# Kernel tuning notes

Hardware: AMD Instinct MI355X
Metric: run time of the kernel (lower is better)

## Reference

```python
import jax, jax.numpy as jnp
import numpy as np

EPS = 1e-05

def exp_map_at_origin(v, c):
    sqrt_c = jnp.sqrt(c)
    v_norm = jnp.maximum(jnp.linalg.norm(v, axis=-1, keepdims=True), EPS)
    return (1.0 / sqrt_c) * jnp.tanh(sqrt_c * v_norm) * (v / v_norm)

def log_map_at_origin(y, c):
    sqrt_c = jnp.sqrt(c)
    y_norm = jnp.maximum(jnp.linalg.norm(y, axis=-1, keepdims=True), EPS)
    y_norm_clamped = jnp.minimum(y_norm, 1.0 / sqrt_c - EPS)
    return (1.0 / sqrt_c) * jnp.arctanh(sqrt_c * y_norm_clamped) * (y / y_norm)

def poincare_distance(x, y, c):
    # x, y: [B, H, S, d]; returns [B, H, S, S]
    sqrt_c = jnp.sqrt(c)
    xns = jnp.sum(x * x, axis=-1, keepdims=True)          # [B,H,S,1]
    yns = jnp.sum(y * y, axis=-1, keepdims=True)          # [B,H,S,1]
    xy = jnp.einsum('bhsd,bhtd->bhst', x, y)
    xnsb = xns                                            # broadcast over t
    ynsb = jnp.swapaxes(yns, -2, -1)                      # [B,H,1,S]
    diff_norm_sq = xnsb - 2.0 * xy + ynsb
    denom = jnp.maximum((1.0 - c * xnsb) * (1.0 - c * ynsb), EPS)
    arg = jnp.maximum(1.0 + 2.0 * c * diff_norm_sq / denom, 1.0 + EPS)
    return (1.0 / sqrt_c) * jnp.arccosh(arg)

def setup_inputs() -> dict:
    key = jax.random.key(0)
    ks = jax.random.split(key, 5)
    B, S, D = 2, 1024, 1024
    x = jax.random.normal(ks[0], (B, S, D), dtype=jnp.float32)
    scale = 0.02
    W_q = scale * jax.random.normal(ks[1], (D, D), dtype=jnp.float32)
    W_k = scale * jax.random.normal(ks[2], (D, D), dtype=jnp.float32)
    W_v = scale * jax.random.normal(ks[3], (D, D), dtype=jnp.float32)
    W_o = scale * jax.random.normal(ks[4], (D, D), dtype=jnp.float32)
    return {
        'x': x, 'W_q': W_q, 'W_k': W_k, 'W_v': W_v, 'W_o': W_o,
        'log_c': jnp.zeros((), jnp.float32),
        'beta': jnp.zeros((), jnp.float32),
        'attention_bias': jnp.zeros((), jnp.float32),
    }

def reference(x, W_q, W_k, W_v, W_o, log_c, beta, attention_bias):
    B, S, D = x.shape
    H = 16
    dh = D // H
    c = jax.nn.softplus(log_c)
    beta_pos = jax.nn.softplus(beta)

    def split_heads(t):  # [B,S,D] -> [B,H,S,dh]
        return jnp.transpose(t.reshape(B, S, H, dh), (0, 2, 1, 3))

    q_t = split_heads(x @ W_q.T)
    k_t = split_heads(x @ W_k.T)
    v_t = split_heads(x @ W_v.T)

    q_h = exp_map_at_origin(q_t, c)
    k_h = exp_map_at_origin(k_t, c)
    v_h = exp_map_at_origin(v_t, c)

    dist = poincare_distance(q_h, k_h, c)                 # [B,H,S,S]
    scores = -beta_pos * dist - attention_bias
    weights = jax.nn.softmax(scores, axis=-1)

    v_tan = log_map_at_origin(v_h, c)
    out_tan = jnp.einsum('bhst,bhtd->bhsd', weights, v_tan)
    out_hyp = exp_map_at_origin(out_tan, c)
    out_heads_tan = log_map_at_origin(out_hyp, c)

    concat = jnp.transpose(out_heads_tan, (0, 2, 1, 3)).reshape(B, S, D)
    return concat @ W_o.T
```

## Files before the change

kernel.cpp:

```cpp
#include <hip/hip_runtime.h>
#include <math.h>


#define EPS_ 1e-5f

constexpr int Ss = 1024, Dd = 1024, Hh = 16, DHh = 64;

typedef __attribute__((ext_vector_type(8))) short bf16x8;
typedef __attribute__((ext_vector_type(4))) short s16x4;
typedef __attribute__((ext_vector_type(4))) float f32x4;

__device__ __forceinline__ float softplusf_(float x) {
    return (x > 20.f) ? x : log1pf(expf(x));
}
__device__ __forceinline__ short f2bf(float f) {
    union { float f; unsigned u; } v; v.f = f;
    unsigned r = v.u + 0x7FFFu + ((v.u >> 16) & 1u);
    return (short)(r >> 16);
}
__device__ __forceinline__ unsigned pks(short a, short b) {
    return (unsigned)(unsigned short)a | ((unsigned)(unsigned short)b << 16);
}

#if __has_builtin(__builtin_amdgcn_cvt_pk_bf16_f32)
typedef __attribute__((ext_vector_type(2))) __bf16 bfp2;
__device__ __forceinline__ unsigned cvtpk(float a, float b) {
    union { bfp2 v; unsigned u; } x;
    x.v = __builtin_amdgcn_cvt_pk_bf16_f32(a, b);
    return x.u;
}
#else
__device__ __forceinline__ unsigned cvtpk(float a, float b) { return pks(f2bf(a), f2bf(b)); }
#endif

#if __has_builtin(__builtin_amdgcn_sqrtf)
#define FSQRT __builtin_amdgcn_sqrtf
#else
#define FSQRT sqrtf
#endif
#if __has_builtin(__builtin_amdgcn_logf)
#define FLOG2 __builtin_amdgcn_logf
#else
#define FLOG2 __log2f
#endif
#if __has_builtin(__builtin_amdgcn_exp2f)
#define FEXP2 __builtin_amdgcn_exp2f
#else
#define FEXP2 exp2f
#endif

__device__ __forceinline__ void gload_lds16(const short* gp, short* lp) {
    __builtin_amdgcn_global_load_lds(
        (__attribute__((address_space(1))) void*)(void*)(const_cast<short*>(gp)),
        (__attribute__((address_space(3))) void*)(void*)(lp), 16, 0, 0);
}

__global__ __launch_bounds__(256) void split_all(
    const float* __restrict__ x,  const float* __restrict__ Wq,
    const float* __restrict__ Wk, const float* __restrict__ Wv,
    const float* __restrict__ Wo,
    short* __restrict__ xh,  short* __restrict__ wqh,
    short* __restrict__ wkh, short* __restrict__ wvh, short* __restrict__ woh)
{
    int g = blockIdx.x * 256 + threadIdx.x;
    const float* src; short* dst; int base;
    if (g < 524288)       { src = x;  dst = xh;  base = g; }
    else if (g < 786432)  { src = Wq; dst = wqh; base = g - 524288; }
    else if (g < 1048576) { src = Wk; dst = wkh; base = g - 786432; }
    else if (g < 1310720) { src = Wv; dst = wvh; base = g - 1048576; }
    else                  { src = Wo; dst = woh; base = g - 1310720; }
    float4 v = *(const float4*)(src + (size_t)base * 4);
    uint2 hp; hp.x = cvtpk(v.x, v.y); hp.y = cvtpk(v.z, v.w);
    *(uint2*)(dst + (size_t)base * 4) = hp;
}

__global__ __launch_bounds__(256, 3) void gemm_qkv(
    const short* __restrict__ Ap,
    const short* __restrict__ Wq, const short* __restrict__ Wk, const short* __restrict__ Wv,
    short* __restrict__ qh, short* __restrict__ kh, short* __restrict__ vtT,
    float* __restrict__ qnsT, float2* __restrict__ knpk,
    const float* __restrict__ p_logc)
{
    const int z = blockIdx.z;
    const short* Bp = (z == 0) ? Wq : (z == 1 ? Wk : Wv);
    const int K = 1024;

    __shared__ short As[128 * 64];
    __shared__ short Bs[64 * 64];

    const int tid = threadIdx.x;
    const int wv = tid >> 6, lane = tid & 63, quad = lane >> 4, l15 = lane & 15;
    const int bm = blockIdx.y * 128, bn = blockIdx.x * 64;

    const int lr8 = lane >> 3, lc8 = lane & 7;
    const int swz8 = (lc8 ^ lr8) * 8;

    const short* gAl = Ap + (size_t)(bm + lr8) * K + swz8;
    const short* gBl = Bp + (size_t)(bn + lr8) * K + swz8;

    f32x4 acc[2][4];
#pragma unroll
    for (int mt = 0; mt < 2; mt++)
#pragma unroll
        for (int j = 0; j < 4; j++) acc[mt][j] = (f32x4){0.f, 0.f, 0.f, 0.f};

    for (int k0 = 0; k0 < K; k0 += 64) {
        __syncthreads();
#pragma unroll
        for (int i = 0; i < 4; i++)
            gload_lds16(gAl + (size_t)((wv * 4 + i) * 8) * K + k0, &As[(wv * 4 + i) * 512]);
#pragma unroll
        for (int j = 0; j < 2; j++)
            gload_lds16(gBl + (size_t)((wv * 2 + j) * 8) * K + k0, &Bs[(wv * 2 + j) * 512]);
        __syncthreads();
#pragma unroll
        for (int w = 0; w < 2; w++) {
            const int xs = ((w * 4 + quad) ^ (l15 & 7)) * 8;
            bf16x8 fa0 = *(const bf16x8*)&As[(wv * 32 + l15) * 64 + xs];
            bf16x8 fa1 = *(const bf16x8*)&As[(wv * 32 + 16 + l15) * 64 + xs];
#pragma unroll
            for (int nt = 0; nt < 4; nt++) {
                bf16x8 fb = *(const bf16x8*)&Bs[(nt * 16 + l15) * 64 + xs];
                acc[0][nt] = __builtin_amdgcn_mfma_f32_16x16x32_bf16(fa0, fb, acc[0][nt], 0, 0, 0);
                acc[1][nt] = __builtin_amdgcn_mfma_f32_16x16x32_bf16(fa1, fb, acc[1][nt], 0, 0, 0);
            }
        }
    }

    const float c = softplusf_(p_logc[0]);
    const float sc = sqrtf(c);
    const float twoC = 2.f * c;
    const int h0 = blockIdx.x;

    if (z < 2) {
        short* yout = (z == 0) ? qh : kh;
#pragma unroll
        for (int mt = 0; mt < 2; mt++) {
            const int mbase = bm + wv * 32 + mt * 16;
            float fr[4];
#pragma unroll
            for (int r = 0; r < 4; r++) {
                float s2 = 0.f;
#pragma unroll
                for (int nt = 0; nt < 4; nt++) s2 += acc[mt][nt][r] * acc[mt][nt][r];
#pragma unroll
                for (int mk = 1; mk < 16; mk <<= 1) s2 += __shfl_xor(s2, mk, 64);
                float n = fmaxf(sqrtf(s2), EPS_);
                float fac = tanhf(sc * n) / (sc * n);
                fr[r] = fac;
                if (l15 == 0) {
                    int m = mbase + quad * 4 + r;
                    int bI = m >> 10, s = m & 1023;
                    float yns = s2 * fac * fac;
                    if (z == 0) {
                        qnsT[(size_t)(bI * Hh + h0) * Ss + s] = yns;
                    } else {
                        knpk[(size_t)(bI * Hh + h0) * Ss + s]
                            = make_float2(yns, twoC / (1.f - c * yns));
                    }
                }
            }
#pragma unroll
            for (int nt = 0; nt < 4; nt++)
#pragma unroll
                for (int r = 0; r < 4; r++) {
                    int m = mbase + quad * 4 + r;
                    yout[(size_t)m * Dd + bn + nt * 16 + l15] = f2bf(acc[mt][nt][r] * fr[r]);
                }
        }
    } else {
#pragma unroll
        for (int mt = 0; mt < 2; mt++) {
            const int mbase = bm + wv * 32 + mt * 16;
            float tr[4];
#pragma unroll
            for (int r = 0; r < 4; r++) {
                float s2 = 0.f;
#pragma unroll
                for (int nt = 0; nt < 4; nt++) s2 += acc[mt][nt][r] * acc[mt][nt][r];
#pragma unroll
                for (int mk = 1; mk < 16; mk <<= 1) s2 += __shfl_xor(s2, mk, 64);
                float n = fmaxf(sqrtf(s2), EPS_);
                float fac = tanhf(sc * n) / (sc * n);
                float yn = n * fac;
                float ycl = fminf(yn, 1.f / sc - EPS_);
                float f2 = atanhf(sc * ycl) / (sc * fmaxf(yn, EPS_));
                tr[r] = fac * f2;
            }
            const int m0 = mbase + quad * 4;
            const int bI = m0 >> 10, s0 = m0 & 1023;
            const int w6 = s0 & 63;
            const int s0p = (s0 & ~63)
                          | ((w6 >> 5) * 32 + ((w6 & 15) >> 2) * 8 + ((w6 >> 4) & 1) * 4);
#pragma unroll
            for (int nt = 0; nt < 4; nt++) {
                int d = nt * 16 + l15;
                uint2 pk;
                pk.x = cvtpk(acc[mt][nt][0] * tr[0], acc[mt][nt][1] * tr[1]);
                pk.y = cvtpk(acc[mt][nt][2] * tr[2], acc[mt][nt][3] * tr[3]);
                *(uint2*)&vtT[((size_t)(bI * Hh + h0) * DHh + d) * Ss + s0p] = pk;
            }
        }
    }
}

__global__ __launch_bounds__(512) void attn_mfma(
    const short* __restrict__ qh, const short* __restrict__ kh, const short* __restrict__ vtT,
    const float* __restrict__ qnsT, const float2* __restrict__ knpk,
    short* __restrict__ ccb,
    const float* __restrict__ p_logc, const float* __restrict__ p_beta)
{
    const float c = softplusf_(p_logc[0]);
    const float sc = sqrtf(c);
    const float bp = softplusf_(p_beta[0]);
    const float nkc = -bp / sc;
    const float cap = 2.f * c * 1e5f;
    const float onePlus = 1.f + EPS_;

    const int bh = blockIdx.x, qt = blockIdx.y;
    const int b = bh >> 4, h = bh & 15;
    const int tid = threadIdx.x;
    const int wv = tid >> 6, lane = tid & 63;
    const int g = wv >> 2, w4 = wv & 3;
    const int quad = lane >> 4, l15 = lane & 15;
    const int q = qt * 64 + w4 * 16 + l15;

    __shared__ short Ks[2][2][4096];
    __shared__ short Vt[2][2][4096];

    const short* qb = qh + (size_t)(b * Ss + q) * Dd + h * DHh + quad * 8;
    bf16x8 qf0 = *(const bf16x8*)qb;
    bf16x8 qf1 = *(const bf16x8*)(qb + 32);

    const float qn = qnsT[(size_t)bh * Ss + q];
    const float irq = 1.f / (1.f - c * qn);

    f32x4 O4[4];
#pragma unroll
    for (int nt = 0; nt < 4; nt++) O4[nt] = (f32x4){0.f, 0.f, 0.f, 0.f};
    float lac = 0.f;

    const int tbase = g * 512;
    const int lr8 = lane >> 3, lc8 = lane & 7;
    const float2* nb = knpk + (size_t)bh * Ss;
    const short* ksb = kh + (size_t)b * Ss * Dd + h * DHh + (lc8 ^ lr8) * 8;
    const short* vsb = vtT + (size_t)bh * DHh * Ss + tbase + (lc8 ^ lr8) * 8;

#pragma unroll
    for (int j = 0; j < 2; j++) {
        const int R = w4 * 16 + j * 8;
        gload_lds16(ksb + (size_t)(tbase + R + lr8) * Dd, &Ks[g][0][R * 64]);
        gload_lds16(vsb + (size_t)(R + lr8) * Ss, &Vt[g][0][R * 64]);
    }
    __syncthreads();

    const int xsl = (quad ^ (l15 & 7)) * 8;

    for (int ch = 0; ch < 8; ch++) {
        const int cur = ch & 1, nxt = cur ^ 1;
        const int t0 = tbase + ch * 64;

        f32x4 n0[4], n1[4];
#pragma unroll
        for (int nt = 0; nt < 4; nt++) {
            const float2* np = nb + t0 + nt * 16 + quad * 4;
            n0[nt] = *(const f32x4*)np;
            n1[nt] = *(const f32x4*)(np + 2);
        }

        f32x4 acc[4];
        __builtin_amdgcn_s_setprio(1);
#pragma unroll
        for (int nt = 0; nt < 4; nt++) {
            bf16x8 k0 = *(const bf16x8*)&Ks[g][cur][(nt * 16 + l15) * 64 + xsl];
            bf16x8 k1 = *(const bf16x8*)&Ks[g][cur][(nt * 16 + l15) * 64 + (xsl ^ 32)];
            f32x4 a = (f32x4){0.f, 0.f, 0.f, 0.f};
            a = __builtin_amdgcn_mfma_f32_16x16x32_bf16(k0, qf0, a, 0, 0, 0);
            a = __builtin_amdgcn_mfma_f32_16x16x32_bf16(k1, qf1, a, 0, 0, 0);
            acc[nt] = a;
        }
        __builtin_amdgcn_s_setprio(0);

        bf16x8 v0[4], v1[4];
#pragma unroll
        for (int nt = 0; nt < 4; nt++) {
            v0[nt] = *(const bf16x8*)&Vt[g][cur][(nt * 16 + l15) * 64 + xsl];
            v1[nt] = *(const bf16x8*)&Vt[g][cur][(nt * 16 + l15) * 64 + (xsl ^ 32)];
        }

        if (ch < 7) {
#pragma unroll
            for (int j = 0; j < 2; j++) {
                const int R = w4 * 16 + j * 8;
                gload_lds16(ksb + (size_t)(tbase + (ch + 1) * 64 + R + lr8) * Dd,
                            &Ks[g][nxt][R * 64]);
                gload_lds16(vsb + (size_t)(R + lr8) * Ss + (ch + 1) * 64,
                            &Vt[g][nxt][R * 64]);
            }
        }

        float sv[4][4];
#pragma unroll
        for (int nt = 0; nt < 4; nt++) {
#pragma unroll
            for (int r = 0; r < 4; r++) {
                float kn   = (r < 2) ? n0[nt][(r & 1) * 2]     : n1[nt][(r & 1) * 2];
                float ik2c = (r < 2) ? n0[nt][(r & 1) * 2 + 1] : n1[nt][(r & 1) * 2 + 1];
                float dns = (qn + kn) - 2.f * acc[nt][r];
                float co  = fminf(irq * ik2c, cap);
                float arg = fmaxf(fmaf(co, dns, 1.f), onePlus);
                float u   = arg + FSQRT(fmaf(arg, arg, -1.f));
                float p   = FEXP2(nkc * FLOG2(u));
                sv[nt][r] = p;
                lac += p;
            }
        }

        union { unsigned u[4]; bf16x8 v; } p0, p1;
        p0.u[0] = cvtpk(sv[0][0], sv[0][1]); p0.u[1] = cvtpk(sv[0][2], sv[0][3]);
        p0.u[2] = cvtpk(sv[1][0], sv[1][1]); p0.u[3] = cvtpk(sv[1][2], sv[1][3]);
        p1.u[0] = cvtpk(sv[2][0], sv[2][1]); p1.u[1] = cvtpk(sv[2][2], sv[2][3]);
        p1.u[2] = cvtpk(sv[3][0], sv[3][1]); p1.u[3] = cvtpk(sv[3][2], sv[3][3]);

        __builtin_amdgcn_s_setprio(1);
#pragma unroll
        for (int nt = 0; nt < 4; nt++) {
            O4[nt] = __builtin_amdgcn_mfma_f32_16x16x32_bf16(v0[nt], p0.v, O4[nt], 0, 0, 0);
            O4[nt] = __builtin_amdgcn_mfma_f32_16x16x32_bf16(v1[nt], p1.v, O4[nt], 0, 0, 0);
        }
        __builtin_amdgcn_s_setprio(0);

        if (ch < 7) __syncthreads();
    }

    lac += __shfl_xor(lac, 16, 64);
    lac += __shfl_xor(lac, 32, 64);

    float* Ored = (float*)&Ks[0][0][0];
    float* lred = (float*)&Vt[0][0][0];
    __syncthreads();
    if (g == 1) {
#pragma unroll
        for (int nt = 0; nt < 4; nt++)
#pragma unroll
            for (int r = 0; r < 4; r++)
                Ored[((w4 * 4 + nt) * 16 + (quad * 4 + r)) * 16 + l15] = O4[nt][r];
        if (lane < 16) lred[w4 * 16 + lane] = lac;
    }
    __syncthreads();

    if (g == 0) {
        const float lt = lac + lred[w4 * 16 + l15];
        const float il = 1.f / lt;
        float ot[4][4], t2 = 0.f;
#pragma unroll
        for (int nt = 0; nt < 4; nt++)
#pragma unroll
            for (int r = 0; r < 4; r++) {
                float v = (O4[nt][r]
                    + Ored[((w4 * 4 + nt) * 16 + (quad * 4 + r)) * 16 + l15]) * il;
                ot[nt][r] = v;
                t2 += v * v;
            }
        t2 += __shfl_xor(t2, 16, 64);
        t2 += __shfl_xor(t2, 32, 64);

        float n = fmaxf(sqrtf(t2), EPS_);
        float fac = tanhf(sc * n) / (sc * n);
        float y2 = t2 * fac * fac;
        float yn = fmaxf(sqrtf(y2), EPS_);
        float ycl = fminf(yn, 1.f / sc - EPS_);
        float fac2 = atanhf(sc * ycl) / (sc * yn);
        float tot = fac * fac2;

        short* ob = ccb + (size_t)(b * Ss + q) * Dd + h * DHh;
#pragma unroll
        for (int nt = 0; nt < 4; nt++) {
            uint2 pk;
            pk.x = cvtpk(ot[nt][0] * tot, ot[nt][1] * tot);
            pk.y = cvtpk(ot[nt][2] * tot, ot[nt][3] * tot);
            *(uint2*)(ob + nt * 16 + quad * 4) = pk;
        }
    }
}

__global__ __launch_bounds__(256, 6) void gemm_out(
    const short* __restrict__ Ap, const short* __restrict__ Bp,
    float* __restrict__ Cp)
{
    const int K = 1024, N = 1024;
    __shared__ short As[64 * 64];
    __shared__ short Bs[64 * 64];
    const int tid = threadIdx.x;
    const int wv = tid >> 6, lane = tid & 63, quad = lane >> 4, l15 = lane & 15;
    const int bm = blockIdx.y * 64, bn = blockIdx.x * 64;

    const int lr8 = lane >> 3, lc8 = lane & 7;
    const int swz8 = (lc8 ^ lr8) * 8;

    const short* gAl = Ap + (size_t)(bm + lr8) * K + swz8;
    const short* gBl = Bp + (size_t)(bn + lr8) * K + swz8;

    f32x4 acc[4];
#pragma unroll
    for (int j = 0; j < 4; j++) acc[j] = (f32x4){0.f, 0.f, 0.f, 0.f};

    for (int k0 = 0; k0 < K; k0 += 64) {
        __syncthreads();
#pragma unroll
        for (int j = 0; j < 2; j++) {
            gload_lds16(gAl + (size_t)((wv * 2 + j) * 8) * K + k0, &As[(wv * 2 + j) * 512]);
            gload_lds16(gBl + (size_t)((wv * 2 + j) * 8) * K + k0, &Bs[(wv * 2 + j) * 512]);
        }
        __syncthreads();
#pragma unroll
        for (int w = 0; w < 2; w++) {
            const int xs = ((w * 4 + quad) ^ (l15 & 7)) * 8;
            bf16x8 fa = *(const bf16x8*)&As[(wv * 16 + l15) * 64 + xs];
#pragma unroll
            for (int nt = 0; nt < 4; nt++) {
                bf16x8 fb = *(const bf16x8*)&Bs[(nt * 16 + l15) * 64 + xs];
                acc[nt] = __builtin_amdgcn_mfma_f32_16x16x32_bf16(fa, fb, acc[nt], 0, 0, 0);
            }
        }
    }
#pragma unroll
    for (int nt = 0; nt < 4; nt++)
#pragma unroll
        for (int r = 0; r < 4; r++)
            Cp[(size_t)(bm + wv * 16 + quad * 4 + r) * N + bn + nt * 16 + l15] = acc[nt][r];
}

extern "C" void kernel_launch(void* const* d_in, const int* in_sizes, int n_in,
                              void* d_out, int out_size, void* d_ws, size_t ws_size,
                              hipStream_t stream)
{
    const float* x    = (const float*)d_in[0];
    const float* Wq   = (const float*)d_in[1];
    const float* Wk   = (const float*)d_in[2];
    const float* Wv   = (const float*)d_in[3];
    const float* Wo   = (const float*)d_in[4];
    const float* logc = (const float*)d_in[5];
    const float* beta = (const float*)d_in[6];
    float* out = (float*)d_out;

    const size_t M2 = 2097152, M1 = 1048576;
    short* ws    = (short*)d_ws;
    short* xh    = ws;
    short* wqh   = xh + M2;
    short* wkh   = wqh + M1;
    short* wvh   = wkh + M1;
    short* woh   = wvh + M1;
    short* qh    = woh + M1;
    short* kh    = qh + M2;
    short* vtT   = kh + M2;
    float* qnsT  = (float*)(vtT + M2);
    float2* knpk = (float2*)(qnsT + 32768);
    short* ccb   = xh;

    split_all<<<dim3(6144), 256, 0, stream>>>(x, Wq, Wk, Wv, Wo, xh, wqh, wkh, wvh, woh);
    gemm_qkv<<<dim3(16, 16, 3), 256, 0, stream>>>(xh, wqh, wkh, wvh,
        qh, kh, vtT, qnsT, knpk, logc);
    attn_mfma<<<dim3(32, 16, 1), 512, 0, stream>>>(qh, kh, vtT, qnsT, knpk,
        ccb, logc, beta);
    gemm_out<<<dim3(16, 32), 256, 0, stream>>>(ccb, woh, out);
}
```

Baseline: 155.4 us.

## Prefetch K/V two chunks ahead and register-double-buffer key norms

Restructures the attention inner loop so K and V tiles are loaded from LDS into registers at the start of each chunk, followed by a barrier. The freed buffer is then refilled with the chunk two steps ahead, which deepens the global-to-LDS prefetch distance. Key-norm values for the next chunk are prefetched into alternating register sets, and the loop is fully unrolled. This aims to hide global memory latency better, in exchange for higher register pressure and the barrier moving earlier in each iteration.

```diff
diff --git a/kernel.cpp b/kernel.cpp
--- a/kernel.cpp
+++ b/kernel.cpp
@@ -246,56 +246,71 @@
     const short* ksb = kh + (size_t)b * Ss * Dd + h * DHh + (lc8 ^ lr8) * 8;
     const short* vsb = vtT + (size_t)bh * DHh * Ss + tbase + (lc8 ^ lr8) * 8;
 
+    f32x4 nA0[4], nA1[4], nB0[4], nB1[4];
+
 #pragma unroll
     for (int j = 0; j < 2; j++) {
         const int R = w4 * 16 + j * 8;
         gload_lds16(ksb + (size_t)(tbase + R + lr8) * Dd, &Ks[g][0][R * 64]);
         gload_lds16(vsb + (size_t)(R + lr8) * Ss, &Vt[g][0][R * 64]);
+        gload_lds16(ksb + (size_t)(tbase + 64 + R + lr8) * Dd, &Ks[g][1][R * 64]);
+        gload_lds16(vsb + (size_t)(R + lr8) * Ss + 64, &Vt[g][1][R * 64]);
+    }
+#pragma unroll
+    for (int nt = 0; nt < 4; nt++) {
+        const float2* np = nb + tbase + nt * 16 + quad * 4;
+        nA0[nt] = *(const f32x4*)np;
+        nA1[nt] = *(const f32x4*)(np + 2);
     }
     __syncthreads();
 
     const int xsl = (quad ^ (l15 & 7)) * 8;
 
+#pragma unroll
     for (int ch = 0; ch < 8; ch++) {
-        const int cur = ch & 1, nxt = cur ^ 1;
-        const int t0 = tbase + ch * 64;
-
-        f32x4 n0[4], n1[4];
-#pragma unroll
-        for (int nt = 0; nt < 4; nt++) {
-            const float2* np = nb + t0 + nt * 16 + quad * 4;
-            n0[nt] = *(const f32x4*)np;
-            n1[nt] = *(const f32x4*)(np + 2);
+        const int cur = ch & 1;
+
+        bf16x8 k0[4], k1[4], v0[4], v1[4];
+#pragma unroll
+        for (int nt = 0; nt < 4; nt++) {
+            k0[nt] = *(const bf16x8*)&Ks[g][cur][(nt * 16 + l15) * 64 + xsl];
+            k1[nt] = *(const bf16x8*)&Ks[g][cur][(nt * 16 + l15) * 64 + (xsl ^ 32)];
+        }
+#pragma unroll
+        for (int nt = 0; nt < 4; nt++) {
+            v0[nt] = *(const bf16x8*)&Vt[g][cur][(nt * 16 + l15) * 64 + xsl];
+            v1[nt] = *(const bf16x8*)&Vt[g][cur][(nt * 16 + l15) * 64 + (xsl ^ 32)];
         }
 
         f32x4 acc[4];
         __builtin_amdgcn_s_setprio(1);
 #pragma unroll
         for (int nt = 0; nt < 4; nt++) {
-            bf16x8 k0 = *(const bf16x8*)&Ks[g][cur][(nt * 16 + l15) * 64 + xsl];
-            bf16x8 k1 = *(const bf16x8*)&Ks[g][cur][(nt * 16 + l15) * 64 + (xsl ^ 32)];
             f32x4 a = (f32x4){0.f, 0.f, 0.f, 0.f};
-            a = __builtin_amdgcn_mfma_f32_16x16x32_bf16(k0, qf0, a, 0, 0, 0);
-            a = __builtin_amdgcn_mfma_f32_16x16x32_bf16(k1, qf1, a, 0, 0, 0);
+            a = __builtin_amdgcn_mfma_f32_16x16x32_bf16(k0[nt], qf0, a, 0, 0, 0);
+            a = __builtin_amdgcn_mfma_f32_16x16x32_bf16(k1[nt], qf1, a, 0, 0, 0);
             acc[nt] = a;
         }
         __builtin_amdgcn_s_setprio(0);
 
-        bf16x8 v0[4], v1[4];
-#pragma unroll
-        for (int nt = 0; nt < 4; nt++) {
-            v0[nt] = *(const bf16x8*)&Vt[g][cur][(nt * 16 + l15) * 64 + xsl];
-            v1[nt] = *(const bf16x8*)&Vt[g][cur][(nt * 16 + l15) * 64 + (xsl ^ 32)];
-        }
-
-        if (ch < 7) {
+        if (ch < 7) __syncthreads();
+
+        if (ch + 2 < 8) {
 #pragma unroll
             for (int j = 0; j < 2; j++) {
                 const int R = w4 * 16 + j * 8;
-                gload_lds16(ksb + (size_t)(tbase + (ch + 1) * 64 + R + lr8) * Dd,
-                            &Ks[g][nxt][R * 64]);
-                gload_lds16(vsb + (size_t)(R + lr8) * Ss + (ch + 1) * 64,
-                            &Vt[g][nxt][R * 64]);
+                gload_lds16(ksb + (size_t)(tbase + (ch + 2) * 64 + R + lr8) * Dd,
+                            &Ks[g][cur][R * 64]);
+                gload_lds16(vsb + (size_t)(R + lr8) * Ss + (ch + 2) * 64,
+                            &Vt[g][cur][R * 64]);
+            }
+        }
+        if (ch + 1 < 8) {
+#pragma unroll
+            for (int nt = 0; nt < 4; nt++) {
+                const float2* np = nb + tbase + (ch + 1) * 64 + nt * 16 + quad * 4;
+                if ((ch & 1) == 0) { nB0[nt] = *(const f32x4*)np; nB1[nt] = *(const f32x4*)(np + 2); }
+                else               { nA0[nt] = *(const f32x4*)np; nA1[nt] = *(const f32x4*)(np + 2); }
             }
         }
 
@@ -304,8 +319,14 @@
         for (int nt = 0; nt < 4; nt++) {
 #pragma unroll
             for (int r = 0; r < 4; r++) {
-                float kn   = (r < 2) ? n0[nt][(r & 1) * 2]     : n1[nt][(r & 1) * 2];
-                float ik2c = (r < 2) ? n0[nt][(r & 1) * 2 + 1] : n1[nt][(r & 1) * 2 + 1];
+                float kn, ik2c;
+                if ((ch & 1) == 0) {
+                    kn   = (r < 2) ? nA0[nt][(r & 1) * 2]     : nA1[nt][(r & 1) * 2];
+                    ik2c = (r < 2) ? nA0[nt][(r & 1) * 2 + 1] : nA1[nt][(r & 1) * 2 + 1];
+                } else {
+                    kn   = (r < 2) ? nB0[nt][(r & 1) * 2]     : nB1[nt][(r & 1) * 2];
+                    ik2c = (r < 2) ? nB0[nt][(r & 1) * 2 + 1] : nB1[nt][(r & 1) * 2 + 1];
+                }
                 float dns = (qn + kn) - 2.f * acc[nt][r];
                 float co  = fminf(irq * ik2c, cap);
                 float arg = fmaxf(fmaf(co, dns, 1.f), onePlus);
@@ -329,8 +350,6 @@
             O4[nt] = __builtin_amdgcn_mfma_f32_16x16x32_bf16(v1[nt], p1.v, O4[nt], 0, 0, 0);
         }
         __builtin_amdgcn_s_setprio(0);
-
-        if (ch < 7) __syncthreads();
     }
 
     lac += __shfl_xor(lac, 16, 64);
```

New measurement: 156.0 us (median of 2 runs). No clear change (+0.4%).
